# Kernel optimization log

Measured on AMD Instinct MI355X. Metric: run time of the kernel, lower is better.

The kernel has to match this reference:

```python
import jax, jax.numpy as jnp
import numpy as np

N, B, K, D = 500000, 100000, 10, 128  # nodes, batch, sampled neighbors, feat dim


def setup_inputs() -> dict:
    key = jax.random.key(0)
    k1, k2, k3, k4 = jax.random.split(key, 4)
    features = jax.random.normal(k1, (N, D), dtype=jnp.float32)
    nodes = jax.random.randint(k2, (B,), 0, N)
    neigh_idx = jax.random.randint(k3, (B, K), 0, N)
    perm = jax.random.permutation(k4, N)  # row shuffle of the embedding matrix
    return {"features": features, "nodes": nodes, "neigh_idx": neigh_idx, "perm": perm}


def reference(features, nodes, neigh_idx, perm):
    # Shuffled embedding matrix (the 'l1' branch permutes rows of embed_matrix)
    shuf_features = features[perm]                      # [N, D]
    # Row-normalized sparse mask @ embed == mean over sampled neighbors
    to_feats = jnp.mean(features[neigh_idx], axis=1)         # [B, D]
    shuf_to_feats = jnp.mean(shuf_features[neigh_idx], axis=1)  # [B, D]
    # mask_self @ embed == gather own node's row
    skip_feats = features[nodes]                             # [B, D]
    shuf_skip_feats = shuf_features[nodes]                   # [B, D]
    return (to_feats, shuf_to_feats, skip_feats, shuf_skip_feats)
```

## Files before the change

### kernel.cpp

```cpp
#include <hip/hip_runtime.h>


using f32x4 = __attribute__((ext_vector_type(4))) float;

template <int K, int D>
__global__ __launch_bounds__(256, 4) void mean_agg_kernel(
    const float* __restrict__ features,
    const int* __restrict__ nodes,
    const int* __restrict__ neigh_idx,
    const int* __restrict__ perm,
    float* __restrict__ out,
    int B) {
  const int row = (blockIdx.x << 3) + (threadIdx.x >> 5);
  if (row >= B) return;
  const int d = (threadIdx.x & 31) << 2;

  int idx[K + 1];
#pragma unroll
  for (int k = 0; k < K; ++k)
    idx[k] = __builtin_nontemporal_load(neigh_idx + row * K + k);
  idx[K] = __builtin_nontemporal_load(nodes + row);

  int pidx[K + 1];
#pragma unroll
  for (int k = 0; k <= K; ++k) pidx[k] = perm[idx[k]];

  f32x4 acc  = {0.f, 0.f, 0.f, 0.f};
  f32x4 sacc = {0.f, 0.f, 0.f, 0.f};
#pragma unroll
  for (int k = 0; k < K; ++k) {
    const f32x4 f  = *reinterpret_cast<const f32x4*>(features + (size_t)idx[k]  * D + d);
    const f32x4 sf = *reinterpret_cast<const f32x4*>(features + (size_t)pidx[k] * D + d);
    acc  += f;
    sacc += sf;
  }
  const f32x4 skip  = *reinterpret_cast<const f32x4*>(features + (size_t)idx[K]  * D + d);
  const f32x4 sskip = *reinterpret_cast<const f32x4*>(features + (size_t)pidx[K] * D + d);

  const float inv = 1.0f / (float)K;
  acc  *= inv;
  sacc *= inv;

  const size_t bd   = (size_t)B * D;
  const size_t base = (size_t)row * D + d;
  __builtin_nontemporal_store(acc,   reinterpret_cast<f32x4*>(out + 0 * bd + base));
  __builtin_nontemporal_store(sacc,  reinterpret_cast<f32x4*>(out + 1 * bd + base));
  __builtin_nontemporal_store(skip,  reinterpret_cast<f32x4*>(out + 2 * bd + base));
  __builtin_nontemporal_store(sskip, reinterpret_cast<f32x4*>(out + 3 * bd + base));
}

extern "C" void kernel_launch(void* const* d_in, const int* in_sizes, int n_in,
                              void* d_out, int out_size, void* d_ws, size_t ws_size,
                              hipStream_t stream) {
  const float* features  = (const float*)d_in[0];
  const int*   nodes     = (const int*)d_in[1];
  const int*   neigh_idx = (const int*)d_in[2];
  const int*   perm      = (const int*)d_in[3];
  float*       out       = (float*)d_out;

  const int B = in_sizes[1];

  const int rowsPerBlock = 8;
  const int grid = (B + rowsPerBlock - 1) / rowsPerBlock;
  mean_agg_kernel<10, 128><<<grid, 256, 0, stream>>>(
      features, nodes, neigh_idx, perm, out, B);
}
```

Measured before the change: 510.8 us.

## Convert features to bf16 in workspace and gather from the half-size copy

Adds a pre-pass that converts the whole fp32 feature table to bf16 (round to nearest even) in the workspace. A new gather kernel then reads 16-byte bf16 chunks per thread (8 values) and accumulates in fp32, with 16 rows per block. The aim is to halve the bytes moved by the random row gathers, which dominate the cost. In exchange every call pays a full streaming pass over the table (read fp32, write bf16). The gathered skip rows, which should be exact copies, now carry bf16 rounding error. The original fp32 kernel stays as a fallback when the workspace is too small.

```diff
diff --git a/kernel.cpp b/kernel.cpp
--- a/kernel.cpp
+++ b/kernel.cpp
@@ -2,9 +2,95 @@
 
 
 using f32x4 = __attribute__((ext_vector_type(4))) float;
+using u16x8 = __attribute__((ext_vector_type(8))) unsigned short;
+
+static __device__ __forceinline__ unsigned short f2bf_rne(float f) {
+  unsigned int u = __builtin_bit_cast(unsigned int, f);
+  u = (u + 0x7FFFu + ((u >> 16) & 1u)) >> 16;
+  return (unsigned short)u;
+}
+static __device__ __forceinline__ float bf2f(unsigned short b) {
+  return __builtin_bit_cast(float, ((unsigned int)b) << 16);
+}
+
+__global__ __launch_bounds__(256) void convert_bf16_kernel(
+    const float* __restrict__ src, unsigned short* __restrict__ dst) {
+  const long long i = ((long long)blockIdx.x * 256 + threadIdx.x) * 8;
+  const f32x4 a = __builtin_nontemporal_load(reinterpret_cast<const f32x4*>(src + i));
+  const f32x4 b = __builtin_nontemporal_load(reinterpret_cast<const f32x4*>(src + i + 4));
+  u16x8 o;
+  o[0] = f2bf_rne(a[0]); o[1] = f2bf_rne(a[1]);
+  o[2] = f2bf_rne(a[2]); o[3] = f2bf_rne(a[3]);
+  o[4] = f2bf_rne(b[0]); o[5] = f2bf_rne(b[1]);
+  o[6] = f2bf_rne(b[2]); o[7] = f2bf_rne(b[3]);
+  *reinterpret_cast<u16x8*>(dst + i) = o;
+}
 
 template <int K, int D>
-__global__ __launch_bounds__(256, 4) void mean_agg_kernel(
+__global__ __launch_bounds__(256, 4) void gather_bf16_kernel(
+    const unsigned short* __restrict__ bf,
+    const int* __restrict__ nodes,
+    const int* __restrict__ neigh_idx,
+    const int* __restrict__ perm,
+    float* __restrict__ out,
+    int B) {
+  const int row = (blockIdx.x << 4) + (threadIdx.x >> 4);
+  if (row >= B) return;
+  const int d = (threadIdx.x & 15) << 3;
+
+  int idx[K + 1];
+#pragma unroll
+  for (int k = 0; k < K; ++k)
+    idx[k] = __builtin_nontemporal_load(neigh_idx + row * K + k);
+  idx[K] = __builtin_nontemporal_load(nodes + row);
+
+  int pidx[K + 1];
+#pragma unroll
+  for (int k = 0; k <= K; ++k) pidx[k] = perm[idx[k]];
+
+  float acc[8] = {0.f, 0.f, 0.f, 0.f, 0.f, 0.f, 0.f, 0.f};
+  float sacc[8] = {0.f, 0.f, 0.f, 0.f, 0.f, 0.f, 0.f, 0.f};
+#pragma unroll
+  for (int k = 0; k < K; ++k) {
+    const u16x8 v  = *reinterpret_cast<const u16x8*>(bf + (size_t)idx[k]  * D + d);
+    const u16x8 sv = *reinterpret_cast<const u16x8*>(bf + (size_t)pidx[k] * D + d);
+#pragma unroll
+    for (int j = 0; j < 8; ++j) {
+      acc[j]  += bf2f(v[j]);
+      sacc[j] += bf2f(sv[j]);
+    }
+  }
+  const u16x8 kv  = *reinterpret_cast<const u16x8*>(bf + (size_t)idx[K]  * D + d);
+  const u16x8 skv = *reinterpret_cast<const u16x8*>(bf + (size_t)pidx[K] * D + d);
+
+  const float inv = 1.0f / (float)K;
+  f32x4 o0a, o0b, o1a, o1b, o2a, o2b, o3a, o3b;
+#pragma unroll
+  for (int j = 0; j < 4; ++j) {
+    o0a[j] = acc[j] * inv;      o0b[j] = acc[j + 4] * inv;
+    o1a[j] = sacc[j] * inv;     o1b[j] = sacc[j + 4] * inv;
+    o2a[j] = bf2f(kv[j]);       o2b[j] = bf2f(kv[j + 4]);
+    o3a[j] = bf2f(skv[j]);      o3b[j] = bf2f(skv[j + 4]);
+  }
+
+  const size_t bd   = (size_t)B * D;
+  const size_t base = (size_t)row * D + d;
+  float* p0 = out + 0 * bd + base;
+  float* p1 = out + 1 * bd + base;
+  float* p2 = out + 2 * bd + base;
+  float* p3 = out + 3 * bd + base;
+  __builtin_nontemporal_store(o0a, reinterpret_cast<f32x4*>(p0));
+  __builtin_nontemporal_store(o0b, reinterpret_cast<f32x4*>(p0 + 4));
+  __builtin_nontemporal_store(o1a, reinterpret_cast<f32x4*>(p1));
+  __builtin_nontemporal_store(o1b, reinterpret_cast<f32x4*>(p1 + 4));
+  __builtin_nontemporal_store(o2a, reinterpret_cast<f32x4*>(p2));
+  __builtin_nontemporal_store(o2b, reinterpret_cast<f32x4*>(p2 + 4));
+  __builtin_nontemporal_store(o3a, reinterpret_cast<f32x4*>(p3));
+  __builtin_nontemporal_store(o3b, reinterpret_cast<f32x4*>(p3 + 4));
+}
+
+template <int K, int D>
+__global__ __launch_bounds__(256, 4) void mean_agg_f32_kernel(
     const float* __restrict__ features,
     const int* __restrict__ nodes,
     const int* __restrict__ neigh_idx,
@@ -25,20 +111,18 @@
 #pragma unroll
   for (int k = 0; k <= K; ++k) pidx[k] = perm[idx[k]];
 
-  f32x4 acc  = {0.f, 0.f, 0.f, 0.f};
+  f32x4 acc = {0.f, 0.f, 0.f, 0.f};
   f32x4 sacc = {0.f, 0.f, 0.f, 0.f};
 #pragma unroll
   for (int k = 0; k < K; ++k) {
-    const f32x4 f  = *reinterpret_cast<const f32x4*>(features + (size_t)idx[k]  * D + d);
-    const f32x4 sf = *reinterpret_cast<const f32x4*>(features + (size_t)pidx[k] * D + d);
-    acc  += f;
-    sacc += sf;
+    acc  += *reinterpret_cast<const f32x4*>(features + (size_t)idx[k]  * D + d);
+    sacc += *reinterpret_cast<const f32x4*>(features + (size_t)pidx[k] * D + d);
   }
   const f32x4 skip  = *reinterpret_cast<const f32x4*>(features + (size_t)idx[K]  * D + d);
   const f32x4 sskip = *reinterpret_cast<const f32x4*>(features + (size_t)pidx[K] * D + d);
 
   const float inv = 1.0f / (float)K;
-  acc  *= inv;
+  acc *= inv;
   sacc *= inv;
 
   const size_t bd   = (size_t)B * D;
@@ -58,10 +142,19 @@
   const int*   perm      = (const int*)d_in[3];
   float*       out       = (float*)d_out;
 
+  const long long ND = in_sizes[0];
   const int B = in_sizes[1];
 
-  const int rowsPerBlock = 8;
-  const int grid = (B + rowsPerBlock - 1) / rowsPerBlock;
-  mean_agg_kernel<10, 128><<<grid, 256, 0, stream>>>(
-      features, nodes, neigh_idx, perm, out, B);
+  if (ws_size >= (size_t)ND * sizeof(unsigned short)) {
+    unsigned short* bf = (unsigned short*)d_ws;
+    const int cgrid = (int)(ND / (256 * 8));
+    convert_bf16_kernel<<<cgrid, 256, 0, stream>>>(features, bf);
+    const int grid = (B + 15) / 16;
+    gather_bf16_kernel<10, 128><<<grid, 256, 0, stream>>>(
+        bf, nodes, neigh_idx, perm, out, B);
+  } else {
+    const int grid = (B + 7) / 8;
+    mean_agg_f32_kernel<10, 128><<<grid, 256, 0, stream>>>(
+        features, nodes, neigh_idx, perm, out, B);
+  }
 }
```

Measured after the change: 506.5 us. About the same (-0.8%).
